# Optimization experiments

Measured on AMD Instinct MI355X. Metric: run time of the kernel, lower is better.

The kernel has to match this reference:

```python
import jax, jax.numpy as jnp
import numpy as np

INV_DELTA = 15.0  # init kwarg inv_delta
EPS = 1e-12       # torch F.normalize eps


def setup_inputs() -> dict:
    key = jax.random.key(0)
    k1, k2 = jax.random.split(key)
    features = jax.random.normal(k1, (32, 256, 30, 30), dtype=jnp.float32)
    # _embedding buffer: randn clamped to >= 0
    embedding = jnp.maximum(jax.random.normal(k2, (2048, 256), dtype=jnp.float32), 0.0)
    # _min_distance_mean buffer, initialized to 0.5
    min_distance_mean = jnp.ones((1,), dtype=jnp.float32) * 0.5
    return {"features": features, "embedding": embedding,
            "min_distance_mean": min_distance_mean}


def reference(features, embedding, min_distance_mean):
    # crop 1-pixel border: [B,C,H,W] -> [B,C,H-2,W-2]
    f = features[:, :, 1:-1, 1:-1]
    # squared euclidean distance to each codeword via GEMM trick:
    # dist[b,k,h,w] = ||f[b,:,h,w]||^2 + ||e[k]||^2 - 2 <f, e[k]>
    f2 = jnp.sum(f * f, axis=1, keepdims=True)                 # [B,1,H',W']
    e2 = jnp.sum(embedding * embedding, axis=1)                # [K]
    xe = jnp.einsum('bchw,kc->bkhw', f, embedding)             # 1x1-conv GEMM
    dist = f2 + e2[None, :, None, None] - 2.0 * xe             # [B,K,H',W']
    # adaptive temperature softmax over codewords
    inv_delta_adaptive = INV_DELTA / min_distance_mean[0]
    codes = jax.nn.softmax(-inv_delta_adaptive * dist, axis=1)  # [B,K,H',W']
    # global average pool + L1 normalize
    bow = jnp.mean(codes, axis=(2, 3))                          # [B,K]
    bow = bow / jnp.maximum(jnp.sum(jnp.abs(bow), axis=1, keepdims=True), EPS)
    return (bow, codes)
```

## Files before the change

kernel.cpp:

```cpp
#include <hip/hip_runtime.h>
#include <hip/hip_bf16.h>
#include <math.h>

typedef __attribute__((ext_vector_type(8))) short bf16x8;
typedef __attribute__((ext_vector_type(16))) float f32x16;

#define B_ 32
#define C_ 256
#define K_ 2048
#define HW_ 784
#define NPIX 25088
#define FEAT_BSTRIDE 230400
#define FEAT_CSTRIDE 900
#define INV_DELTA 15.0f
#define LOG2E 1.4426950408889634f
#define QSCALE 409.6f
#define QDEC (LOG2E / QSCALE)

#define BM 128
#define BN 128
#define BKC 32
#define NCH 8
#define NSLAB 16

#define AS1 __attribute__((address_space(1)))
#define AS3 __attribute__((address_space(3)))

__device__ __forceinline__ ushort f2bf(float x) {
    __hip_bfloat16 h = __float2bfloat16(x);
    return *reinterpret_cast<ushort*>(&h);
}
__device__ __forceinline__ float bf2f(ushort u) {
    __hip_bfloat16 h;
    *reinterpret_cast<ushort*>(&h) = u;
    return __bfloat162float(h);
}
__device__ __forceinline__ void gl_lds16(const ushort* g, ushort* l) {
    __builtin_amdgcn_global_load_lds((AS1 const uint*)g, (AS3 uint*)l, 16, 0, 0);
}

__global__ void e2_kernel(const float* __restrict__ emb, float* __restrict__ e2) {
    int t = threadIdx.x;
    int wid = t >> 6, lane = t & 63;
    int k = blockIdx.x * 4 + wid;
    const float* er = emb + (size_t)k * C_;
    float v0 = er[lane], v1 = er[lane + 64], v2 = er[lane + 128], v3 = er[lane + 192];
    float s = v0 * v0 + v1 * v1 + v2 * v2 + v3 * v3;
#pragma unroll
    for (int off = 32; off > 0; off >>= 1) s += __shfl_xor(s, off);
    if (lane == 0) e2[k] = s;
}

__global__ void prep_e_kernel(const float* __restrict__ emb,
                              ushort* __restrict__ ehi, ushort* __restrict__ elo) {
    int i = blockIdx.x * 256 + threadIdx.x;
    float v = emb[i];
    ushort h = f2bf(v);
    float r = v - bf2f(h);
    ehi[i] = h;
    elo[i] = f2bf(r);
}

__global__ __launch_bounds__(256) void prep_f_kernel(const float* __restrict__ feat,
                                                     ushort* __restrict__ fhi,
                                                     ushort* __restrict__ flo) {
    __shared__ float F[256 * 65];
    int t = threadIdx.x;
    int px0 = blockIdx.x * 64;
    {
        int lane = t & 63, cq = t >> 6;
        int px = px0 + lane;
        int b = px / HW_, hw = px % HW_;
        int h = hw / 28, w = hw % 28;
        const float* base = feat + (size_t)b * FEAT_BSTRIDE + (size_t)(h + 1) * 30 + (w + 1);
#pragma unroll
        for (int cc = 0; cc < 64; ++cc) {
            int c = cq * 64 + cc;
            F[c * 65 + lane] = base[(size_t)c * FEAT_CSTRIDE];
        }
    }
    __syncthreads();
    {
        int px_l = t >> 2, cseg = t & 3;
        size_t ob = (size_t)(px0 + px_l) * C_ + cseg * 64;
        uint uh[32], ul[32];
#pragma unroll
        for (int j = 0; j < 32; ++j) {
            float v0 = F[(cseg * 64 + 2 * j) * 65 + px_l];
            float v1 = F[(cseg * 64 + 2 * j + 1) * 65 + px_l];
            ushort h0 = f2bf(v0), h1 = f2bf(v1);
            float r0 = v0 - bf2f(h0), r1 = v1 - bf2f(h1);
            uh[j] = (uint)h0 | ((uint)h1 << 16);
            ul[j] = (uint)f2bf(r0) | ((uint)f2bf(r1) << 16);
        }
#pragma unroll
        for (int j = 0; j < 8; ++j) {
            *reinterpret_cast<uint4*>(&fhi[ob + j * 8]) = *reinterpret_cast<uint4*>(&uh[j * 4]);
            *reinterpret_cast<uint4*>(&flo[ob + j * 8]) = *reinterpret_cast<uint4*>(&ul[j * 4]);
        }
    }
}

__global__ __launch_bounds__(256, 3) void gemm_kernel(
    const ushort* __restrict__ fhi, const ushort* __restrict__ flo,
    const ushort* __restrict__ ehi, const ushort* __restrict__ elo,
    const float* __restrict__ mdm, const float* __restrict__ e2g,
    ushort* __restrict__ zq, float* __restrict__ m_part, float* __restrict__ l_part)
{
    __shared__ __align__(16) ushort Fsmem[2][2][BM * BKC];
    __shared__ float redA[2][132];
    __shared__ float redM[132];

    int t = threadIdx.x;
    int lane = t & 63, wid = t >> 6;
    int wrow = wid >> 1, wcol = wid & 1;
    int g = lane >> 5, ci = lane & 31;

    int bid = blockIdx.x;
    int swz = (bid & 7) * 392 + (bid >> 3);
    int tile = swz >> 4, slab = swz & 15;
    int px0 = tile * BM;
    int k0 = slab * BN;

    auto stageF = [&](int buf, int ch) {
        int c0 = ch * BKC;
#pragma unroll
        for (int i = 0; i < 2; ++i) {
            int p = t + i * 256;
            int rp = p >> 3, q = p & 7;
            int v = q ^ (rp & 7);
            int row = rp * 2 + (v >> 2);
            int cu = (v & 3) * 8;
            size_t ga = (size_t)(px0 + row) * C_ + c0 + cu;
            gl_lds16(fhi + ga, &Fsmem[buf][0][p * 8]);
            gl_lds16(flo + ga, &Fsmem[buf][1][p * 8]);
        }
    };

    const ushort* peh[2];
    const ushort* pel[2];
#pragma unroll
    for (int ni = 0; ni < 2; ++ni) {
        size_t r = (size_t)(k0 + wcol * 64 + ni * 32 + ci) * C_ + g * 8;
        peh[ni] = ehi + r;
        pel[ni] = elo + r;
    }
    bf16x8 ehS[2][2], elS[2][2];
    auto loadE = [&](int slot, int gs) {
        int off = gs * 16;
#pragma unroll
        for (int ni = 0; ni < 2; ++ni) {
            ehS[slot][ni] = *reinterpret_cast<const bf16x8*>(peh[ni] + off);
            elS[slot][ni] = *reinterpret_cast<const bf16x8*>(pel[ni] + off);
        }
    };

    f32x16 acc[2][2];
#pragma unroll
    for (int mi = 0; mi < 2; ++mi)
#pragma unroll
        for (int ni = 0; ni < 2; ++ni)
            acc[mi][ni] = (f32x16)(0.0f);

    int xr = (ci >> 1) & 7;
    int bb4 = (ci & 1) * 4;
    int rpF0 = wrow * 32 + (ci >> 1);

    stageF(0, 0);
    loadE(0, 0);
    asm volatile("s_waitcnt vmcnt(2)" ::: "memory");
    __builtin_amdgcn_s_barrier();

#pragma unroll
    for (int ch = 0; ch < NCH; ++ch) {
        if (ch + 1 < NCH) stageF((ch + 1) & 1, ch + 1);
#pragma unroll
        for (int s = 0; s < 2; ++s) {
            int gs = ch * 2 + s;
            if (gs + 1 < 2 * NCH) loadE((gs + 1) & 1, gs + 1);
            __builtin_amdgcn_sched_barrier(0);
            int qs = (bb4 + s * 2 + g) ^ xr;
            bf16x8 fh[2], fl[2];
#pragma unroll
            for (int mi = 0; mi < 2; ++mi) {
                int off = (rpF0 + mi * 16) * 64 + qs * 8;
                fh[mi] = *reinterpret_cast<const bf16x8*>(&Fsmem[ch & 1][0][off]);
                fl[mi] = *reinterpret_cast<const bf16x8*>(&Fsmem[ch & 1][1][off]);
            }
            int cs = gs & 1;
#pragma unroll
            for (int mi = 0; mi < 2; ++mi)
#pragma unroll
                for (int ni = 0; ni < 2; ++ni) {
                    acc[mi][ni] = __builtin_amdgcn_mfma_f32_32x32x16_bf16(ehS[cs][ni], fh[mi], acc[mi][ni], 0, 0, 0);
                    acc[mi][ni] = __builtin_amdgcn_mfma_f32_32x32x16_bf16(elS[cs][ni], fh[mi], acc[mi][ni], 0, 0, 0);
                    acc[mi][ni] = __builtin_amdgcn_mfma_f32_32x32x16_bf16(ehS[cs][ni], fl[mi], acc[mi][ni], 0, 0, 0);
                }
        }
        if (ch + 1 < NCH) {
            asm volatile("s_waitcnt vmcnt(4)" ::: "memory");
            __builtin_amdgcn_s_barrier();
        }
    }

    const float alpha = INV_DELTA / mdm[0];
    {
        const float* e2b = e2g + k0 + wcol * 64 + 4 * g;
#pragma unroll
        for (int ni = 0; ni < 2; ++ni)
#pragma unroll
            for (int q = 0; q < 4; ++q) {
                float4 ev = *reinterpret_cast<const float4*>(e2b + ni * 32 + 8 * q);
#pragma unroll
                for (int mi = 0; mi < 2; ++mi) {
                    acc[mi][ni][4 * q + 0] = alpha * (2.f * acc[mi][ni][4 * q + 0] - ev.x);
                    acc[mi][ni][4 * q + 1] = alpha * (2.f * acc[mi][ni][4 * q + 1] - ev.y);
                    acc[mi][ni][4 * q + 2] = alpha * (2.f * acc[mi][ni][4 * q + 2] - ev.z);
                    acc[mi][ni][4 * q + 3] = alpha * (2.f * acc[mi][ni][4 * q + 3] - ev.w);
                }
            }
    }

    float mt[2];
#pragma unroll
    for (int mi = 0; mi < 2; ++mi) {
        float m = acc[mi][0][0];
#pragma unroll
        for (int ni = 0; ni < 2; ++ni)
#pragma unroll
            for (int r = 0; r < 16; ++r) m = fmaxf(m, acc[mi][ni][r]);
        m = fmaxf(m, __shfl_xor(m, 32));
        mt[mi] = m;
        if (lane < 32) redA[wcol][wrow * 64 + mi * 32 + ci] = m;
    }
    __syncthreads();
    if (t < 128) redM[t] = fmaxf(redA[0][t], redA[1][t]);
    __syncthreads();
    float ms[2];
#pragma unroll
    for (int mi = 0; mi < 2; ++mi) ms[mi] = redM[wrow * 64 + mi * 32 + ci];

#pragma unroll
    for (int mi = 0; mi < 2; ++mi) {
        float l = 0.f;
#pragma unroll
        for (int ni = 0; ni < 2; ++ni)
#pragma unroll
            for (int r = 0; r < 16; ++r) l += exp2f((acc[mi][ni][r] - ms[mi]) * LOG2E);
        l += __shfl_xor(l, 32);
        if (lane < 32) redA[wcol][wrow * 64 + mi * 32 + ci] = l;
    }
    __syncthreads();
    if (t < 128) {
        m_part[(size_t)slab * NPIX + px0 + t] = redM[t];
        l_part[(size_t)slab * NPIX + px0 + t] = redA[0][t] + redA[1][t];
    }

#pragma unroll
    for (int mi = 0; mi < 2; ++mi) {
        int pxx = px0 + wrow * 64 + mi * 32 + ci;
        int bb = pxx / HW_, hh = pxx - bb * HW_;
        ushort* zb = zq + ((size_t)bb * K_ + (k0 + wcol * 64 + 4 * g)) * HW_ + hh;
#pragma unroll
        for (int ni = 0; ni < 2; ++ni)
#pragma unroll
            for (int q = 0; q < 4; ++q)
#pragma unroll
                for (int j = 0; j < 4; ++j) {
                    float s0 = fmaxf((acc[mi][ni][4 * q + j] - ms[mi]) * QSCALE, -32760.f);
                    short v = (short)(int)s0;
                    zb[(size_t)(ni * 32 + 8 * q + j) * HW_] = (ushort)v;
                }
    }
}

__global__ void combine_kernel(const float* __restrict__ m_part, const float* __restrict__ l_part,
                               float* __restrict__ m_fin, float* __restrict__ rl_g) {
    int p = blockIdx.x * 256 + threadIdx.x;
    float m = -3.4e38f;
#pragma unroll
    for (int s = 0; s < NSLAB; ++s) m = fmaxf(m, m_part[(size_t)s * NPIX + p]);
    float l = 0.f;
#pragma unroll
    for (int s = 0; s < NSLAB; ++s)
        l += l_part[(size_t)s * NPIX + p] * exp2f((m_part[(size_t)s * NPIX + p] - m) * LOG2E);
    m_fin[p] = m;
    rl_g[p] = 1.0f / l;
}

__global__ __launch_bounds__(256) void finish_kernel(
    const ushort* __restrict__ zq, const float* __restrict__ m_part,
    const float* __restrict__ m_fin, const float* __restrict__ rl_g,
    float* __restrict__ codes, float* __restrict__ bow)
{
    __shared__ float corr[HW_], rls[HW_];
    __shared__ float bsum[64][4];
    int t = threadIdx.x;
    int kc = blockIdx.x, b = blockIdx.y;
    int slab = kc >> 1;
    for (int i = t; i < HW_; i += 256) {
        int p = b * HW_ + i;
        corr[i] = (m_part[(size_t)slab * NPIX + p] - m_fin[p]) * LOG2E;
        rls[i] = rl_g[p];
    }
    __syncthreads();
    int wid = t >> 6, lane = t & 63;
    for (int kl = 0; kl < 64; ++kl) {
        int k = kc * 64 + kl;
        size_t base = ((size_t)b * K_ + k) * HW_;
        float ssum = 0.f;
        if (t < 196) {
            uint2 raw = *reinterpret_cast<const uint2*>(&zq[base + t * 4]);
            int q0 = (int)(short)(raw.x & 0xffffu), q1 = (int)(short)(raw.x >> 16);
            int q2 = (int)(short)(raw.y & 0xffffu), q3 = (int)(short)(raw.y >> 16);
            float4 out;
            out.x = exp2f(fmaf((float)q0, QDEC, corr[t * 4 + 0])) * rls[t * 4 + 0];
            out.y = exp2f(fmaf((float)q1, QDEC, corr[t * 4 + 1])) * rls[t * 4 + 1];
            out.z = exp2f(fmaf((float)q2, QDEC, corr[t * 4 + 2])) * rls[t * 4 + 2];
            out.w = exp2f(fmaf((float)q3, QDEC, corr[t * 4 + 3])) * rls[t * 4 + 3];
            *reinterpret_cast<float4*>(&codes[base + t * 4]) = out;
            ssum = out.x + out.y + out.z + out.w;
        }
#pragma unroll
        for (int off = 32; off > 0; off >>= 1) ssum += __shfl_xor(ssum, off);
        if (lane == 0) bsum[kl][wid] = ssum;
    }
    __syncthreads();
    if (t < 64) {
        float s = bsum[t][0] + bsum[t][1] + bsum[t][2] + bsum[t][3];
        bow[(size_t)b * K_ + kc * 64 + t] = s * (1.0f / 784.0f);
    }
}

__global__ void bownorm_kernel(float* __restrict__ bow) {
    __shared__ float wred[4];
    __shared__ float denom_s;
    int b = blockIdx.x, t = threadIdx.x;
    float* row = bow + (size_t)b * K_;
    float v[8];
    float s = 0.f;
#pragma unroll
    for (int i = 0; i < 8; ++i) {
        v[i] = row[t + i * 256];
        s += fabsf(v[i]);
    }
#pragma unroll
    for (int off = 32; off > 0; off >>= 1) s += __shfl_xor(s, off);
    int wid = t >> 6, lane = t & 63;
    if (lane == 0) wred[wid] = s;
    __syncthreads();
    if (t == 0) denom_s = fmaxf(wred[0] + wred[1] + wred[2] + wred[3], 1e-12f);
    __syncthreads();
    float denom = denom_s;
#pragma unroll
    for (int i = 0; i < 8; ++i) row[t + i * 256] = v[i] / denom;
}

extern "C" void kernel_launch(void* const* d_in, const int* in_sizes, int n_in,
                              void* d_out, int out_size, void* d_ws, size_t ws_size,
                              hipStream_t stream) {
    const float* feat = (const float*)d_in[0];
    const float* emb  = (const float*)d_in[1];
    const float* mdm  = (const float*)d_in[2];
    float* bow   = (float*)d_out;
    float* codes = bow + (size_t)B_ * K_;

    char* ws = (char*)d_ws;
    size_t off = 0;
    auto alloc = [&](size_t bytes) { char* p = ws + off; off = (off + bytes + 255) & ~(size_t)255; return p; };
    ushort* ehi    = (ushort*)alloc((size_t)K_ * C_ * 2);
    ushort* elo    = (ushort*)alloc((size_t)K_ * C_ * 2);
    float*  e2     = (float*)alloc(K_ * 4);
    float*  m_part = (float*)alloc((size_t)NSLAB * NPIX * 4);
    float*  l_part = (float*)alloc((size_t)NSLAB * NPIX * 4);
    float*  m_fin  = (float*)alloc((size_t)NPIX * 4);
    float*  rl_g   = (float*)alloc((size_t)NPIX * 4);
    ushort* zq     = (ushort*)alloc((size_t)NPIX * K_ * 2);

    ushort* fhi = (ushort*)codes;
    ushort* flo = fhi + (size_t)NPIX * C_;

    e2_kernel<<<512, 256, 0, stream>>>(emb, e2);
    prep_e_kernel<<<2048, 256, 0, stream>>>(emb, ehi, elo);
    prep_f_kernel<<<392, 256, 0, stream>>>(feat, fhi, flo);
    gemm_kernel<<<3136, 256, 0, stream>>>(fhi, flo, ehi, elo, mdm, e2, zq, m_part, l_part);
    combine_kernel<<<98, 256, 0, stream>>>(m_part, l_part, m_fin, rl_g);
    finish_kernel<<<dim3(32, 32), 256, 0, stream>>>(zq, m_part, m_fin, rl_g, codes, bow);
    bownorm_kernel<<<32, 256, 0, stream>>>(bow);
}
```

Baseline: 229.1 us.

## Load feature operands directly from global into registers, dropping LDS staging

Removes the LDS double-buffered staging of the feature tile (global_load_lds plus barriers). Each wave now loads its feature fragments straight from global memory into registers, software-pipelined alongside the embedding fragments. This removes LDS traffic and block-wide barriers, but the two column waves now each fetch the same feature rows, doubling global/L2 reads. Launch bounds are lowered from 3 to 2 waves per SIMD to make room for the extra registers, which reduces occupancy.

Result: slower. 297.1 us (+29.7%).

```diff
diff --git a/kernel.cpp b/kernel.cpp
--- a/kernel.cpp
+++ b/kernel.cpp
@@ -19,12 +19,7 @@
 
 #define BM 128
 #define BN 128
-#define BKC 32
-#define NCH 8
 #define NSLAB 16
-
-#define AS1 __attribute__((address_space(1)))
-#define AS3 __attribute__((address_space(3)))
 
 __device__ __forceinline__ ushort f2bf(float x) {
     __hip_bfloat16 h = __float2bfloat16(x);
@@ -34,9 +29,6 @@
     __hip_bfloat16 h;
     *reinterpret_cast<ushort*>(&h) = u;
     return __bfloat162float(h);
-}
-__device__ __forceinline__ void gl_lds16(const ushort* g, ushort* l) {
-    __builtin_amdgcn_global_load_lds((AS1 const uint*)g, (AS3 uint*)l, 16, 0, 0);
 }
 
 __global__ void e2_kernel(const float* __restrict__ emb, float* __restrict__ e2) {
@@ -101,13 +93,12 @@
     }
 }
 
-__global__ __launch_bounds__(256, 3) void gemm_kernel(
+__global__ __launch_bounds__(256, 2) void gemm_kernel(
     const ushort* __restrict__ fhi, const ushort* __restrict__ flo,
     const ushort* __restrict__ ehi, const ushort* __restrict__ elo,
     const float* __restrict__ mdm, const float* __restrict__ e2g,
     ushort* __restrict__ zq, float* __restrict__ m_part, float* __restrict__ l_part)
 {
-    __shared__ __align__(16) ushort Fsmem[2][2][BM * BKC];
     __shared__ float redA[2][132];
     __shared__ float redM[132];
 
@@ -122,32 +113,38 @@
     int px0 = tile * BM;
     int k0 = slab * BN;
 
-    auto stageF = [&](int buf, int ch) {
-        int c0 = ch * BKC;
-#pragma unroll
-        for (int i = 0; i < 2; ++i) {
-            int p = t + i * 256;
-            int rp = p >> 3, q = p & 7;
-            int v = q ^ (rp & 7);
-            int row = rp * 2 + (v >> 2);
-            int cu = (v & 3) * 8;
-            size_t ga = (size_t)(px0 + row) * C_ + c0 + cu;
-            gl_lds16(fhi + ga, &Fsmem[buf][0][p * 8]);
-            gl_lds16(flo + ga, &Fsmem[buf][1][p * 8]);
-        }
-    };
-
+    const ushort* pfh[2];
+    const ushort* pfl[2];
     const ushort* peh[2];
     const ushort* pel[2];
+#pragma unroll
+    for (int mi = 0; mi < 2; ++mi) {
+        size_t r = (size_t)(px0 + wrow * 64 + mi * 32 + ci) * C_ + g * 8;
+        pfh[mi] = fhi + r;
+        pfl[mi] = flo + r;
+    }
 #pragma unroll
     for (int ni = 0; ni < 2; ++ni) {
         size_t r = (size_t)(k0 + wcol * 64 + ni * 32 + ci) * C_ + g * 8;
         peh[ni] = ehi + r;
         pel[ni] = elo + r;
     }
-    bf16x8 ehS[2][2], elS[2][2];
-    auto loadE = [&](int slot, int gs) {
-        int off = gs * 16;
+
+    f32x16 acc[2][2];
+#pragma unroll
+    for (int mi = 0; mi < 2; ++mi)
+#pragma unroll
+        for (int ni = 0; ni < 2; ++ni)
+            acc[mi][ni] = (f32x16)(0.0f);
+
+    bf16x8 fhS[2][2], flS[2][2], ehS[2][2], elS[2][2];
+    auto ldf = [&](int slot, int s) {
+        int off = s * 16;
+#pragma unroll
+        for (int mi = 0; mi < 2; ++mi) {
+            fhS[slot][mi] = *reinterpret_cast<const bf16x8*>(pfh[mi] + off);
+            flS[slot][mi] = *reinterpret_cast<const bf16x8*>(pfl[mi] + off);
+        }
 #pragma unroll
         for (int ni = 0; ni < 2; ++ni) {
             ehS[slot][ni] = *reinterpret_cast<const bf16x8*>(peh[ni] + off);
@@ -155,52 +152,22 @@
         }
     };
 
-    f32x16 acc[2][2];
-#pragma unroll
-    for (int mi = 0; mi < 2; ++mi)
-#pragma unroll
-        for (int ni = 0; ni < 2; ++ni)
-            acc[mi][ni] = (f32x16)(0.0f);
-
-    int xr = (ci >> 1) & 7;
-    int bb4 = (ci & 1) * 4;
-    int rpF0 = wrow * 32 + (ci >> 1);
-
-    stageF(0, 0);
-    loadE(0, 0);
-    asm volatile("s_waitcnt vmcnt(2)" ::: "memory");
-    __builtin_amdgcn_s_barrier();
-
-#pragma unroll
-    for (int ch = 0; ch < NCH; ++ch) {
-        if (ch + 1 < NCH) stageF((ch + 1) & 1, ch + 1);
-#pragma unroll
-        for (int s = 0; s < 2; ++s) {
-            int gs = ch * 2 + s;
-            if (gs + 1 < 2 * NCH) loadE((gs + 1) & 1, gs + 1);
-            __builtin_amdgcn_sched_barrier(0);
-            int qs = (bb4 + s * 2 + g) ^ xr;
-            bf16x8 fh[2], fl[2];
-#pragma unroll
-            for (int mi = 0; mi < 2; ++mi) {
-                int off = (rpF0 + mi * 16) * 64 + qs * 8;
-                fh[mi] = *reinterpret_cast<const bf16x8*>(&Fsmem[ch & 1][0][off]);
-                fl[mi] = *reinterpret_cast<const bf16x8*>(&Fsmem[ch & 1][1][off]);
+    ldf(0, 0);
+    __builtin_amdgcn_sched_barrier(0);
+#pragma unroll
+    for (int s = 0; s < 16; ++s) {
+        if (s + 1 < 16) ldf((s + 1) & 1, s + 1);
+        __builtin_amdgcn_sched_barrier(0);
+        int cs = s & 1;
+#pragma unroll
+        for (int mi = 0; mi < 2; ++mi)
+#pragma unroll
+            for (int ni = 0; ni < 2; ++ni) {
+                acc[mi][ni] = __builtin_amdgcn_mfma_f32_32x32x16_bf16(ehS[cs][ni], fhS[cs][mi], acc[mi][ni], 0, 0, 0);
+                acc[mi][ni] = __builtin_amdgcn_mfma_f32_32x32x16_bf16(elS[cs][ni], fhS[cs][mi], acc[mi][ni], 0, 0, 0);
+                acc[mi][ni] = __builtin_amdgcn_mfma_f32_32x32x16_bf16(ehS[cs][ni], flS[cs][mi], acc[mi][ni], 0, 0, 0);
             }
-            int cs = gs & 1;
-#pragma unroll
-            for (int mi = 0; mi < 2; ++mi)
-#pragma unroll
-                for (int ni = 0; ni < 2; ++ni) {
-                    acc[mi][ni] = __builtin_amdgcn_mfma_f32_32x32x16_bf16(ehS[cs][ni], fh[mi], acc[mi][ni], 0, 0, 0);
-                    acc[mi][ni] = __builtin_amdgcn_mfma_f32_32x32x16_bf16(elS[cs][ni], fh[mi], acc[mi][ni], 0, 0, 0);
-                    acc[mi][ni] = __builtin_amdgcn_mfma_f32_32x32x16_bf16(ehS[cs][ni], fl[mi], acc[mi][ni], 0, 0, 0);
-                }
-        }
-        if (ch + 1 < NCH) {
-            asm volatile("s_waitcnt vmcnt(4)" ::: "memory");
-            __builtin_amdgcn_s_barrier();
-        }
+        __builtin_amdgcn_sched_barrier(0);
     }
 
     const float alpha = INV_DELTA / mdm[0];
```
